# Optimization experiments

Hardware: AMD Instinct MI355X
Metric: run time of the kernel (lower is better)

Reference implementation:

```python
import jax, jax.numpy as jnp
import numpy as np

B, M, N, DIM = 4, 3, 2048, 512
H = 4
HD = DIM // H  # 128
SCALE = float(np.sqrt(HD))  # code divides scores by sqrt(head_dim)


def setup_inputs() -> dict:
    key = jax.random.key(0)
    ks = jax.random.split(key, 9)
    s = 0.02
    return {
        "query": jax.random.normal(ks[0], (B, M, N, DIM), jnp.float32),
        "key": jax.random.normal(ks[1], (B, M, N, DIM), jnp.float32),
        "value": jax.random.normal(ks[2], (B, M, N, DIM), jnp.float32),
        "Wq": jax.random.normal(ks[3], (DIM, DIM), jnp.float32) * s,
        "bq": jax.random.normal(ks[4], (DIM,), jnp.float32) * s,
        "Wk": jax.random.normal(ks[5], (DIM, DIM), jnp.float32) * s,
        "bk": jax.random.normal(ks[6], (DIM,), jnp.float32) * s,
        "Wv": jax.random.normal(ks[7], (DIM, DIM), jnp.float32) * s,
        "bv": jax.random.normal(ks[8], (DIM,), jnp.float32) * s,
    }


def reference(query, key, value, Wq, bq, Wk, bk, Wv, bv):
    b, m, n, dim = query.shape
    # nn.Linear: x @ W.T + b
    Q = (query @ Wq.T + bq).reshape(b, m, n, H, HD)
    K = (key @ Wk.T + bk).reshape(b, m, n, H, HD)
    V = (value @ Wv.T + bv).reshape(b, m, n, H, HD)
    # scores: [b, m, H, n, n]
    scores = jnp.einsum("bmqhd,bmkhd->bmhqk", Q, K) / SCALE
    attn = jax.nn.softmax(scores, axis=-1)
    out = jnp.einsum("bmhqk,bmkhd->bmqhd", attn, V)
    return out.reshape(b, m, n, dim)
```

## Files before the change

kernel.cpp:

```cpp
#include <hip/hip_runtime.h>
#include <hip/hip_bf16.h>


typedef short s16x8 __attribute__((ext_vector_type(8)));
typedef unsigned short u16x8 __attribute__((ext_vector_type(8)));
typedef float f32x4 __attribute__((ext_vector_type(4)));

#define MFMA16(a, b, c) __builtin_amdgcn_mfma_f32_16x16x32_bf16((a), (b), (c), 0, 0, 0)

static __device__ __forceinline__ unsigned short f2bf(float f) {
    union { float f; unsigned u; } v; v.f = f;
    unsigned r = v.u + 0x7FFFu + ((v.u >> 16) & 1u);
    return (unsigned short)(r >> 16);
}
static __device__ __forceinline__ unsigned pk2(float a, float b) {
    unsigned r;
    asm("v_cvt_pk_bf16_f32 %0, %1, %2" : "=v"(r) : "v"(a), "v"(b));
    return r;
}
static __device__ __forceinline__ float exp2_hw(float x) {
    float r;
    asm("v_exp_f32 %0, %1" : "=v"(r) : "v"(x));
    return r;
}

#define OSTR 72

__global__ __launch_bounds__(256, 2)
void qkv_proj_kernel(const float* __restrict__ Xq, const float* __restrict__ Xk,
                     const float* __restrict__ Xv,
                     const float* __restrict__ Wq, const float* __restrict__ bq,
                     const float* __restrict__ Wk, const float* __restrict__ bk,
                     const float* __restrict__ Wv, const float* __restrict__ bv,
                     unsigned short* __restrict__ ws_q,
                     unsigned short* __restrict__ ws_k,
                     unsigned short* __restrict__ ws_vt)
{
    __shared__ __align__(16) char smem[65536];

    const int which = blockIdx.z;
    const float* X    = (which == 0) ? Xq : (which == 1) ? Xk : Xv;
    const float* W    = (which == 0) ? Wq : (which == 1) ? Wk : Wv;
    const float* bias = (which == 0) ? bq : (which == 1) ? bk : bv;

    const int r0 = blockIdx.x * 128;
    const int c0 = blockIdx.y * 128;
    const int tid = threadIdx.x;
    const int lane = tid & 63, wave = tid >> 6;
    const int l15 = lane & 15, quad = lane >> 4;
    const int wr = (wave >> 1) * 64, wc = (wave & 1) * 64;

    const int srow = tid >> 4;
    const int scol = tid & 15;
    const int cf = scol * 4;
    const int cb = scol * 8;

    f32x4 acc[4][4] = {};

    {
        char* A0 = smem;
        char* B0 = smem + 16384;
        for (int i = 0; i < 8; ++i) {
            const int row = i * 16 + srow;
            float4 fa = *(const float4*)&X[(size_t)(r0 + row) * 512 + cf];
            float4 fb = *(const float4*)&W[(size_t)(c0 + row) * 512 + cf];
            uint2 wa, wb;
            wa.x = pk2(fa.x, fa.y); wa.y = pk2(fa.z, fa.w);
            wb.x = pk2(fb.x, fb.y); wb.y = pk2(fb.z, fb.w);
            const int sw = cb ^ ((row & 7) << 4);
            *(uint2*)(A0 + row * 128 + sw) = wa;
            *(uint2*)(B0 + row * 128 + sw) = wb;
        }
    }
    __syncthreads();

    for (int it = 0; it < 8; ++it) {
        char* Ac = smem + (it & 1) * 32768;
        char* Bc = Ac + 16384;
        const bool pre = (it < 7);

        float4 ra[8], rb[8];
        if (pre) {
            const int kn = (it + 1) * 64;
            for (int i = 0; i < 8; ++i) {
                const int row = i * 16 + srow;
                ra[i] = *(const float4*)&X[(size_t)(r0 + row) * 512 + kn + cf];
                rb[i] = *(const float4*)&W[(size_t)(c0 + row) * 512 + kn + cf];
            }
        }

        for (int kk = 0; kk < 2; ++kk) {
            s16x8 af[4], bf_[4];
            for (int mi = 0; mi < 4; ++mi) {
                const int row = wr + mi * 16 + l15;
                af[mi] = *(const s16x8*)(Ac + row * 128 +
                                         ((kk * 64 + quad * 16) ^ ((row & 7) << 4)));
            }
            for (int ni = 0; ni < 4; ++ni) {
                const int row = wc + ni * 16 + l15;
                bf_[ni] = *(const s16x8*)(Bc + row * 128 +
                                          ((kk * 64 + quad * 16) ^ ((row & 7) << 4)));
            }
            for (int mi = 0; mi < 4; ++mi)
                for (int ni = 0; ni < 4; ++ni)
                    acc[mi][ni] = MFMA16(af[mi], bf_[ni], acc[mi][ni]);
        }

        if (pre) {
            char* An = smem + ((it & 1) ^ 1) * 32768;
            char* Bn = An + 16384;
            for (int i = 0; i < 8; ++i) {
                const int row = i * 16 + srow;
                uint2 wa, wb;
                wa.x = pk2(ra[i].x, ra[i].y); wa.y = pk2(ra[i].z, ra[i].w);
                wb.x = pk2(rb[i].x, rb[i].y); wb.y = pk2(rb[i].z, rb[i].w);
                const int sw = cb ^ ((row & 7) << 4);
                *(uint2*)(An + row * 128 + sw) = wa;
                *(uint2*)(Bn + row * 128 + sw) = wb;
            }
        }
        __syncthreads();
    }

    float bvals[4];
    for (int ni = 0; ni < 4; ++ni) bvals[ni] = bias[c0 + wc + ni * 16 + l15];

    __syncthreads();
    unsigned short* St = (unsigned short*)smem + wave * (64 * OSTR);
    const int h = blockIdx.y;
    const int bm = (r0 + wr) >> 11;
    const int n0 = (r0 + wr) & 2047;

    if (which != 2) {
        for (int mi = 0; mi < 4; ++mi)
            for (int ni = 0; ni < 4; ++ni)
                for (int r = 0; r < 4; ++r)
                    St[(mi * 16 + quad * 4 + r) * OSTR + ni * 16 + l15] =
                        f2bf(acc[mi][ni][r] + bvals[ni]);
        unsigned short* dst = (which == 0) ? ws_q : ws_k;
        for (int p = 0; p < 8; ++p) {
            const int row = p * 8 + (lane >> 3);
            const int coff = (lane & 7) * 8;
            s16x8 v = *(const s16x8*)&St[row * OSTR + coff];
            *(s16x8*)&dst[((size_t)(bm * 4 + h) * 2048 + n0 + row) * 128 + wc + coff] = v;
        }
    } else {
        for (int mi = 0; mi < 4; ++mi)
            for (int ni = 0; ni < 4; ++ni)
                for (int r = 0; r < 4; ++r)
                    St[(ni * 16 + l15) * OSTR + mi * 16 + quad * 4 + r] =
                        f2bf(acc[mi][ni][r] + bvals[ni]);
        for (int p = 0; p < 8; ++p) {
            const int col = p * 8 + (lane >> 3);
            const int roff = (lane & 7) * 8;
            s16x8 v = *(const s16x8*)&St[col * OSTR + roff];
            *(s16x8*)&ws_vt[(((size_t)(bm * 4 + h)) * 128 + wc + col) * 2048 + n0 + roff] = v;
        }
    }
}

#define VSTR 80

__global__ __launch_bounds__(256)
void attn_kernel(const unsigned short* __restrict__ Qw,
                 const unsigned short* __restrict__ Kw,
                 const unsigned short* __restrict__ Vtw,
                 float* __restrict__ out)
{
    __shared__ char lds[36864];
    char* Kb0 = lds;
    char* Kb1 = lds + 8192;
    char* Vb0 = lds + 16384;
    char* Vb1 = lds + 26624;

    const int tid = threadIdx.x, lane = tid & 63, wave = tid >> 6;
    const int l15 = lane & 15, quad = lane >> 4;
    const int q0 = blockIdx.x * 128, h = blockIdx.y, bm = blockIdx.z;

    const unsigned short* Qh = Qw  + (size_t)(bm * 4 + h) * 2048 * 128;
    const unsigned short* Kh = Kw  + (size_t)(bm * 4 + h) * 2048 * 128;
    const unsigned short* Vh = Vtw + (size_t)(bm * 4 + h) * 128 * 2048;

    const int sk_key  = tid >> 3, sk_c   = tid & 7;
    const int sv_hd   = tid >> 1, sv_hlf = tid & 1;
    const int skx = sk_key & 7;
    const int krx = (l15 & 7) << 4;

    s16x8 qf[2][4];
    for (int qh = 0; qh < 2; ++qh)
        for (int kk = 0; kk < 4; ++kk)
            qf[qh][kk] = *(const s16x8*)&Qh[(size_t)(q0 + wave * 32 + qh * 16 + l15) * 128 + kk * 32 + quad * 8];

    {
        u16x8 ka = *(const u16x8*)&Kh[(size_t)sk_key * 128 + sk_c * 16];
        u16x8 kb = *(const u16x8*)&Kh[(size_t)sk_key * 128 + sk_c * 16 + 8];
        u16x8 va = *(const u16x8*)&Vh[(size_t)sv_hd * 2048 + sv_hlf * 16];
        u16x8 vb = *(const u16x8*)&Vh[(size_t)sv_hd * 2048 + sv_hlf * 16 + 8];
        *(u16x8*)(Kb0 + sk_key * 256 + (((sk_c * 2) ^ skx) << 4))     = ka;
        *(u16x8*)(Kb0 + sk_key * 256 + (((sk_c * 2 + 1) ^ skx) << 4)) = kb;
        *(u16x8*)(Vb0 + sv_hd * VSTR + sv_hlf * 32)      = va;
        *(u16x8*)(Vb0 + sv_hd * VSTR + sv_hlf * 32 + 16) = vb;
    }
    __syncthreads();

    f32x4 acc[2][8] = {};
    float rsum[2] = {0.f, 0.f};

    const float CEXP = 1.4426950408889634f / 11.313708498984761f;

    for (int it = 0; it < 64; ++it) {
        const int k0 = it * 32;
        char* Kc = (it & 1) ? Kb1 : Kb0;
        char* Vc = (it & 1) ? Vb1 : Vb0;
        char* Kn = (it & 1) ? Kb0 : Kb1;
        char* Vn = (it & 1) ? Vb0 : Vb1;
        const bool do_stage = (it < 63);

        u16x8 ka, kb, va, vb;
        if (do_stage) {
            const int kn0 = k0 + 32;
            ka = *(const u16x8*)&Kh[(size_t)(kn0 + sk_key) * 128 + sk_c * 16];
            kb = *(const u16x8*)&Kh[(size_t)(kn0 + sk_key) * 128 + sk_c * 16 + 8];
            va = *(const u16x8*)&Vh[(size_t)sv_hd * 2048 + kn0 + sv_hlf * 16];
            vb = *(const u16x8*)&Vh[(size_t)sv_hd * 2048 + kn0 + sv_hlf * 16 + 8];
        }

        f32x4 s[2][2] = {};
        __builtin_amdgcn_s_setprio(1);
        for (int kk = 0; kk < 4; ++kk) {
            s16x8 kf0 = *(const s16x8*)(Kc + l15 * 256        + (((kk * 4 + quad) << 4) ^ krx));
            s16x8 kf1 = *(const s16x8*)(Kc + (16 + l15) * 256 + (((kk * 4 + quad) << 4) ^ krx));
            s[0][0] = MFMA16(kf0, qf[0][kk], s[0][0]);
            s[0][1] = MFMA16(kf1, qf[0][kk], s[0][1]);
            s[1][0] = MFMA16(kf0, qf[1][kk], s[1][0]);
            s[1][1] = MFMA16(kf1, qf[1][kk], s[1][1]);
        }
        __builtin_amdgcn_s_setprio(0);

        s16x8 pf[2];
        for (int qh = 0; qh < 2; ++qh) {
            const float p00 = exp2_hw(s[qh][0][0] * CEXP);
            const float p01 = exp2_hw(s[qh][0][1] * CEXP);
            const float p02 = exp2_hw(s[qh][0][2] * CEXP);
            const float p03 = exp2_hw(s[qh][0][3] * CEXP);
            const float p10 = exp2_hw(s[qh][1][0] * CEXP);
            const float p11 = exp2_hw(s[qh][1][1] * CEXP);
            const float p12 = exp2_hw(s[qh][1][2] * CEXP);
            const float p13 = exp2_hw(s[qh][1][3] * CEXP);
            rsum[qh] += ((p00 + p01) + (p02 + p03)) + ((p10 + p11) + (p12 + p13));
            unsigned x0 = pk2(p00, p01), y0 = pk2(p02, p03);
            unsigned x1 = pk2(p10, p11), y1 = pk2(p12, p13);
            asm("v_permlane32_swap_b32 %0, %1" : "+v"(x0), "+v"(x1));
            asm("v_permlane16_swap_b32 %0, %1" : "+v"(x0), "+v"(x1));
            asm("v_permlane32_swap_b32 %0, %1" : "+v"(y0), "+v"(y1));
            asm("v_permlane16_swap_b32 %0, %1" : "+v"(y0), "+v"(y1));
            union { unsigned u[4]; s16x8 v; } pu;
            pu.u[0] = x0; pu.u[1] = y0; pu.u[2] = x1; pu.u[3] = y1;
            pf[qh] = pu.v;
        }

        __builtin_amdgcn_s_setprio(1);
        for (int mb = 0; mb < 8; ++mb) {
            s16x8 vtf = *(const s16x8*)(Vc + (mb * 16 + l15) * VSTR + quad * 16);
            acc[0][mb] = MFMA16(vtf, pf[0], acc[0][mb]);
            acc[1][mb] = MFMA16(vtf, pf[1], acc[1][mb]);
        }
        __builtin_amdgcn_s_setprio(0);

        if (do_stage) {
            *(u16x8*)(Kn + sk_key * 256 + (((sk_c * 2) ^ skx) << 4))     = ka;
            *(u16x8*)(Kn + sk_key * 256 + (((sk_c * 2 + 1) ^ skx) << 4)) = kb;
            *(u16x8*)(Vn + sv_hd * VSTR + sv_hlf * 32)      = va;
            *(u16x8*)(Vn + sv_hd * VSTR + sv_hlf * 32 + 16) = vb;
        }

        __syncthreads();
    }

    for (int qh = 0; qh < 2; ++qh) {
        rsum[qh] += __shfl_xor(rsum[qh], 16);
        rsum[qh] += __shfl_xor(rsum[qh], 32);
    }
    for (int qh = 0; qh < 2; ++qh) {
        const float inv = 1.f / rsum[qh];
        float* orow = out + ((size_t)bm * 2048 + q0 + wave * 32 + qh * 16 + l15) * 512 + h * 128;
        for (int mb = 0; mb < 8; ++mb) {
            float4 v;
            v.x = acc[qh][mb][0] * inv; v.y = acc[qh][mb][1] * inv;
            v.z = acc[qh][mb][2] * inv; v.w = acc[qh][mb][3] * inv;
            *(float4*)&orow[mb * 16 + quad * 4] = v;
        }
    }
}

extern "C" void kernel_launch(void* const* d_in, const int* in_sizes, int n_in,
                              void* d_out, int out_size, void* d_ws, size_t ws_size,
                              hipStream_t stream) {
    const float* Xq = (const float*)d_in[0];
    const float* Xk = (const float*)d_in[1];
    const float* Xv = (const float*)d_in[2];
    const float* Wq = (const float*)d_in[3];
    const float* bq = (const float*)d_in[4];
    const float* Wk = (const float*)d_in[5];
    const float* bk = (const float*)d_in[6];
    const float* Wv = (const float*)d_in[7];
    const float* bv = (const float*)d_in[8];
    float* out = (float*)d_out;

    unsigned short* ws = (unsigned short*)d_ws;
    const size_t per_tensor = (size_t)12 * 4 * 2048 * 128;
    unsigned short* ws_q  = ws;
    unsigned short* ws_k  = ws + per_tensor;
    unsigned short* ws_vt = ws + 2 * per_tensor;

    qkv_proj_kernel<<<dim3(192, 4, 3), 256, 0, stream>>>(
        Xq, Xk, Xv, Wq, bq, Wk, bk, Wv, bv, ws_q, ws_k, ws_vt);

    attn_kernel<<<dim3(16, 4, 12), 256, 0, stream>>>(ws_q, ws_k, ws_vt, out);
}
```

Baseline: 421.2 us.

## Drop LDS staging in attention; read K/V fragments directly from global with XCD-aware block mapping

Removes the double-buffered LDS staging of K and V tiles and the per-iteration block barrier. Each wave now loads its MFMA fragments straight from global memory and relies on L2/cache reuse across the four waves and across blocks. The block index is remapped so all query tiles of one (batch, head) pair land on the same XCD, which keeps K/V resident in that XCD's L2, and launch bounds request 3 blocks per SIMD. The risk is many redundant, less coalesced global loads (the V fragment loads stride by 2048 elements) and longer load latency in place of LDS reads.

```diff
diff --git a/kernel.cpp b/kernel.cpp
--- a/kernel.cpp
+++ b/kernel.cpp
@@ -159,50 +159,31 @@
     }
 }
 
-#define VSTR 80
-
-__global__ __launch_bounds__(256)
+__global__ __launch_bounds__(256, 3)
 void attn_kernel(const unsigned short* __restrict__ Qw,
                  const unsigned short* __restrict__ Kw,
                  const unsigned short* __restrict__ Vtw,
                  float* __restrict__ out)
 {
-    __shared__ char lds[36864];
-    char* Kb0 = lds;
-    char* Kb1 = lds + 8192;
-    char* Vb0 = lds + 16384;
-    char* Vb1 = lds + 26624;
-
     const int tid = threadIdx.x, lane = tid & 63, wave = tid >> 6;
     const int l15 = lane & 15, quad = lane >> 4;
-    const int q0 = blockIdx.x * 128, h = blockIdx.y, bm = blockIdx.z;
+
+    const int lin = blockIdx.x + 16 * (blockIdx.y + 4 * blockIdx.z);
+    const int xcd = lin & 7, ix = lin >> 3;
+    const int combo = xcd * 6 + (ix >> 4);
+    const int qt = ix & 15;
+    const int h = combo & 3, bm = combo >> 2;
+    const int q0 = qt * 128;
 
     const unsigned short* Qh = Qw  + (size_t)(bm * 4 + h) * 2048 * 128;
     const unsigned short* Kh = Kw  + (size_t)(bm * 4 + h) * 2048 * 128;
     const unsigned short* Vh = Vtw + (size_t)(bm * 4 + h) * 128 * 2048;
-
-    const int sk_key  = tid >> 3, sk_c   = tid & 7;
-    const int sv_hd   = tid >> 1, sv_hlf = tid & 1;
-    const int skx = sk_key & 7;
-    const int krx = (l15 & 7) << 4;
 
     s16x8 qf[2][4];
     for (int qh = 0; qh < 2; ++qh)
         for (int kk = 0; kk < 4; ++kk)
             qf[qh][kk] = *(const s16x8*)&Qh[(size_t)(q0 + wave * 32 + qh * 16 + l15) * 128 + kk * 32 + quad * 8];
 
-    {
-        u16x8 ka = *(const u16x8*)&Kh[(size_t)sk_key * 128 + sk_c * 16];
-        u16x8 kb = *(const u16x8*)&Kh[(size_t)sk_key * 128 + sk_c * 16 + 8];
-        u16x8 va = *(const u16x8*)&Vh[(size_t)sv_hd * 2048 + sv_hlf * 16];
-        u16x8 vb = *(const u16x8*)&Vh[(size_t)sv_hd * 2048 + sv_hlf * 16 + 8];
-        *(u16x8*)(Kb0 + sk_key * 256 + (((sk_c * 2) ^ skx) << 4))     = ka;
-        *(u16x8*)(Kb0 + sk_key * 256 + (((sk_c * 2 + 1) ^ skx) << 4)) = kb;
-        *(u16x8*)(Vb0 + sv_hd * VSTR + sv_hlf * 32)      = va;
-        *(u16x8*)(Vb0 + sv_hd * VSTR + sv_hlf * 32 + 16) = vb;
-    }
-    __syncthreads();
-
     f32x4 acc[2][8] = {};
     float rsum[2] = {0.f, 0.f};
 
@@ -210,26 +191,12 @@
 
     for (int it = 0; it < 64; ++it) {
         const int k0 = it * 32;
-        char* Kc = (it & 1) ? Kb1 : Kb0;
-        char* Vc = (it & 1) ? Vb1 : Vb0;
-        char* Kn = (it & 1) ? Kb0 : Kb1;
-        char* Vn = (it & 1) ? Vb0 : Vb1;
-        const bool do_stage = (it < 63);
-
-        u16x8 ka, kb, va, vb;
-        if (do_stage) {
-            const int kn0 = k0 + 32;
-            ka = *(const u16x8*)&Kh[(size_t)(kn0 + sk_key) * 128 + sk_c * 16];
-            kb = *(const u16x8*)&Kh[(size_t)(kn0 + sk_key) * 128 + sk_c * 16 + 8];
-            va = *(const u16x8*)&Vh[(size_t)sv_hd * 2048 + kn0 + sv_hlf * 16];
-            vb = *(const u16x8*)&Vh[(size_t)sv_hd * 2048 + kn0 + sv_hlf * 16 + 8];
-        }
 
         f32x4 s[2][2] = {};
         __builtin_amdgcn_s_setprio(1);
         for (int kk = 0; kk < 4; ++kk) {
-            s16x8 kf0 = *(const s16x8*)(Kc + l15 * 256        + (((kk * 4 + quad) << 4) ^ krx));
-            s16x8 kf1 = *(const s16x8*)(Kc + (16 + l15) * 256 + (((kk * 4 + quad) << 4) ^ krx));
+            s16x8 kf0 = *(const s16x8*)&Kh[(size_t)(k0 + l15) * 128 + kk * 32 + quad * 8];
+            s16x8 kf1 = *(const s16x8*)&Kh[(size_t)(k0 + 16 + l15) * 128 + kk * 32 + quad * 8];
             s[0][0] = MFMA16(kf0, qf[0][kk], s[0][0]);
             s[0][1] = MFMA16(kf1, qf[0][kk], s[0][1]);
             s[1][0] = MFMA16(kf0, qf[1][kk], s[1][0]);
@@ -261,20 +228,11 @@
 
         __builtin_amdgcn_s_setprio(1);
         for (int mb = 0; mb < 8; ++mb) {
-            s16x8 vtf = *(const s16x8*)(Vc + (mb * 16 + l15) * VSTR + quad * 16);
+            s16x8 vtf = *(const s16x8*)&Vh[(size_t)(mb * 16 + l15) * 2048 + k0 + quad * 8];
             acc[0][mb] = MFMA16(vtf, pf[0], acc[0][mb]);
             acc[1][mb] = MFMA16(vtf, pf[1], acc[1][mb]);
         }
         __builtin_amdgcn_s_setprio(0);
-
-        if (do_stage) {
-            *(u16x8*)(Kn + sk_key * 256 + (((sk_c * 2) ^ skx) << 4))     = ka;
-            *(u16x8*)(Kn + sk_key * 256 + (((sk_c * 2 + 1) ^ skx) << 4)) = kb;
-            *(u16x8*)(Vn + sv_hd * VSTR + sv_hlf * 32)      = va;
-            *(u16x8*)(Vn + sv_hd * VSTR + sv_hlf * 32 + 16) = vb;
-        }
-
-        __syncthreads();
     }
 
     for (int qh = 0; qh < 2; ++qh) {
```

Result: slower. 614.0 us (+45.8%).
